# Kernel tuning notes

Hardware: AMD Instinct MI355X
Metric: run time of the kernel (lower is better)

## Reference

```python
import jax, jax.numpy as jnp
import numpy as np

# SectorAttention (PARTNER): dim=256, resolution=(4,4096), H_sp=4, W_sp=1, H=4, heads=8
B, Hq, Hres, Wres, C, NH = 4, 4, 4, 4096, 256, 8
H_SP, W_SP = 4, 1
HD = C // NH
SCALE = HD ** -0.5


def _forward(s, x, s_pos, x_pos, Wq, bq, Wk, bk, Wv, bv, Wo, bo,
             pw1, pb1, bn_g, bn_b, bn_m, bn_v, pw2, pb2,
             ln_g, ln_b, mw1, mb1, mw2, mb2):
    Bb, Lq, Cc = s.shape
    W = Wres
    nW = Bb * (W // W_SP)
    # ---- dynamic relative-position bias (per-window small conv net) ----
    xp = x_pos.reshape(Bb, Hq // H_SP, H_SP, W // W_SP, W_SP, 2)
    xp = jnp.transpose(xp, (0, 1, 3, 5, 2, 4)).reshape(-1, 2, H_SP * W_SP)   # (nW,2,4)
    sp = jnp.transpose(s_pos, (0, 2, 3, 1)).reshape(-1, 2, Hq * W_SP)        # (nW,2,4)
    rel = sp[:, :, :, None] - xp[:, :, None, :]                              # (nW,2,4,4)
    rel = rel.reshape(nW, 2, -1)                                             # (nW,2,16)
    h = jnp.einsum('oc,bcl->bol', pw1, rel) + pb1[None, :, None]             # Conv1d k=1
    h = (h - bn_m[None, :, None]) * jax.lax.rsqrt(bn_v[None, :, None] + 1e-5) \
        * bn_g[None, :, None] + bn_b[None, :, None]                          # BatchNorm1d (eval)
    h = jax.nn.relu(h)
    h = jnp.einsum('oc,bcl->bol', pw2, h) + pb2[None, :, None]               # Conv1d k=1 -> heads
    rel_bias = h.reshape(-1, NH, Hq, H_SP)                                   # (nW,NH,4,4) since W_SP==1
    # ---- projections + window partitioning ----
    q = s @ Wq.T + bq
    q = q.reshape(Bb, Cc, Hq, W)                          # faithful torch .view reinterpretation
    q = q.reshape(Bb, NH, HD, Hq, W // W_SP, W_SP)
    q = jnp.transpose(q, (0, 4, 1, 3, 5, 2)).reshape(-1, NH, Hq * W_SP, HD)

    def im2cswin(t):
        t = jnp.transpose(t, (0, 2, 1)).reshape(Bb, Cc, Hres, W)
        t = t.reshape(Bb, Cc, Hres // H_SP, H_SP, W // W_SP, W_SP)
        t = jnp.transpose(t, (0, 2, 4, 3, 5, 1)).reshape(-1, H_SP * W_SP, Cc)
        return jnp.transpose(t.reshape(-1, H_SP * W_SP, NH, HD), (0, 2, 1, 3))

    k = im2cswin(x @ Wk.T + bk)
    v = im2cswin(x @ Wv.T + bv)
    # ---- windowed attention with dynamic bias ----
    attn = jnp.einsum('wnqd,wnkd->wnqk', q * SCALE, k) + rel_bias
    attn = jax.nn.softmax(attn, axis=-1)
    o = jnp.einsum('wnqk,wnkd->wnqd', attn, v)            # (nW,NH,4,HD)
    o = jnp.transpose(o, (0, 2, 1, 3)).reshape(-1, Hq * W_SP, Cc)
    # windows2img(o, H_sp=Hq, W_sp=W_SP, H=Hq, W=W)
    o = o.reshape(Bb, Hq // Hq, W // W_SP, Hq, W_SP, Cc)
    o = jnp.transpose(o, (0, 1, 3, 2, 4, 5)).reshape(Bb, Hq * W, Cc)
    o = o @ Wo.T + bo
    s1 = s + o
    # ---- LayerNorm + MLP (residual) ----
    mu = jnp.mean(s1, axis=-1, keepdims=True)
    var = jnp.mean((s1 - mu) ** 2, axis=-1, keepdims=True)
    n = (s1 - mu) * jax.lax.rsqrt(var + 1e-5) * ln_g + ln_b
    h2 = jax.nn.gelu(n @ mw1.T + mb1, approximate=False)
    return s1 + h2 @ mw2.T + mb2


def setup_inputs() -> dict:
    key = jax.random.key(0)
    ks = jax.random.split(key, 12)
    rn = lambda k, sh, sc=1.0: jax.random.normal(k, sh, dtype=jnp.float32) * sc
    H4 = 4 * C
    return {
        's': rn(ks[0], (B, Hq * Wres, C)),
        'x': rn(ks[1], (B, Hres * Wres, C)),
        's_pos': rn(ks[2], (B, 2, Wres // W_SP, Hq * W_SP)),
        'x_pos': rn(ks[3], (B, Hres * Wres, 2)),
        'Wq': rn(ks[4], (C, C), 0.02), 'bq': jnp.zeros((C,), jnp.float32),
        'Wk': rn(ks[5], (C, C), 0.02), 'bk': jnp.zeros((C,), jnp.float32),
        'Wv': rn(ks[6], (C, C), 0.02), 'bv': jnp.zeros((C,), jnp.float32),
        'Wo': rn(ks[7], (C, C), 0.02), 'bo': jnp.zeros((C,), jnp.float32),
        'pw1': rn(ks[8], (16, 2), 0.2), 'pb1': jnp.zeros((16,), jnp.float32),
        'bn_g': jnp.ones((16,), jnp.float32), 'bn_b': jnp.zeros((16,), jnp.float32),
        'bn_m': jnp.zeros((16,), jnp.float32), 'bn_v': jnp.ones((16,), jnp.float32),
        'pw2': rn(ks[9], (NH, 16), 0.2), 'pb2': jnp.zeros((NH,), jnp.float32),
        'ln_g': jnp.ones((C,), jnp.float32), 'ln_b': jnp.zeros((C,), jnp.float32),
        'mw1': rn(ks[10], (H4, C), 0.02), 'mb1': jnp.zeros((H4,), jnp.float32),
        'mw2': rn(ks[11], (C, H4), 0.02), 'mb2': jnp.zeros((C,), jnp.float32),
    }


def reference(s, x, s_pos, x_pos, Wq, bq, Wk, bk, Wv, bv, Wo, bo,
              pw1, pb1, bn_g, bn_b, bn_m, bn_v, pw2, pb2,
              ln_g, ln_b, mw1, mb1, mw2, mb2):
    return _forward(s, x, s_pos, x_pos, Wq, bq, Wk, bk, Wv, bv, Wo, bo,
                    pw1, pb1, bn_g, bn_b, bn_m, bn_v, pw2, pb2,
                    ln_g, ln_b, mw1, mb1, mw2, mb2)
```

## Files before the change

kernel.cpp:

```cpp
#include <hip/hip_runtime.h>
#include <hip/hip_bf16.h>
#include <math.h>

typedef __hip_bfloat16 BF;
typedef __bf16 bf16x8 __attribute__((ext_vector_type(8)));
typedef float f32x4 __attribute__((ext_vector_type(4)));

struct alignas(8) BF4 { BF v[4]; };
struct alignas(16) BF8 { BF v[8]; };

static __device__ __forceinline__ float b2f(BF x) { return __bfloat162float(x); }
static __device__ __forceinline__ BF f2b(float x) { return __float2bfloat16(x); }

static __device__ __forceinline__ void gld_lds16(const void* g, void* l) {
  __builtin_amdgcn_global_load_lds(
      (const __attribute__((address_space(1))) unsigned int*)g,
      (__attribute__((address_space(3))) unsigned int*)l, 16, 0, 0);
}

__global__ void __launch_bounds__(256) cvt_kernel(
    const float* __restrict__ in, BF* __restrict__ out, int n4) {
  for (int i = blockIdx.x * 256 + threadIdx.x; i < n4; i += gridDim.x * 256) {
    float4 v = ((const float4*)in)[i];
    BF4 o;
    o.v[0] = f2b(v.x); o.v[1] = f2b(v.y); o.v[2] = f2b(v.z); o.v[3] = f2b(v.w);
    ((BF4*)out)[i] = o;
  }
}

__global__ void __launch_bounds__(256) bkv_kernel(
    const float* __restrict__ bk, const float* __restrict__ bv,
    float* __restrict__ bkv) {
  int i = blockIdx.x * 256 + threadIdx.x;
  bkv[i] = (i < 256) ? bk[i] : bv[i - 256];
}

__global__ void __launch_bounds__(256) bias_kernel(
    const float* __restrict__ s_pos, const float* __restrict__ x_pos,
    const float* __restrict__ pw1, const float* __restrict__ pb1,
    const float* __restrict__ bn_g, const float* __restrict__ bn_b,
    const float* __restrict__ bn_m, const float* __restrict__ bn_v,
    const float* __restrict__ pw2, const float* __restrict__ pb2,
    float* __restrict__ out) {
  int gid = blockIdx.x * 256 + threadIdx.x;
  int w = gid >> 4, l = gid & 15;
  int b = w >> 12, wi = w & 4095;
  int i = l >> 2, j = l & 3;
  int e0 = i, e1 = 4 + i;
  float sp0 = s_pos[(((size_t)b * 2 + (e0 & 1)) * 4096 + wi) * 4 + (e0 >> 1)];
  float sp1 = s_pos[(((size_t)b * 2 + (e1 & 1)) * 4096 + wi) * 4 + (e1 >> 1)];
  float xp0 = x_pos[((size_t)b * 16384 + j * 4096 + wi) * 2 + 0];
  float xp1 = x_pos[((size_t)b * 16384 + j * 4096 + wi) * 2 + 1];
  float r0 = sp0 - xp0, r1 = sp1 - xp1;
  float acc[8];
#pragma unroll
  for (int p = 0; p < 8; ++p) acc[p] = pb2[p];
#pragma unroll
  for (int o = 0; o < 16; ++o) {
    float t = pw1[o * 2 + 0] * r0 + pw1[o * 2 + 1] * r1 + pb1[o];
    float sc = bn_g[o] / sqrtf(bn_v[o] + 1e-5f);
    t = (t - bn_m[o]) * sc + bn_b[o];
    t = fmaxf(t, 0.0f);
#pragma unroll
    for (int p = 0; p < 8; ++p) acc[p] += pw2[p * 16 + o] * t;
  }
#pragma unroll
  for (int p = 0; p < 8; ++p) out[(size_t)w * 128 + p * 16 + l] = acc[p];
}

enum { EPI_NONE = 0, EPI_RES = 1, EPI_GELU = 2 };

template <int EPI, typename AT, typename RT, typename CT>
__global__ void __launch_bounds__(256, 2) gemm_tn(
    const AT* __restrict__ A, const BF* __restrict__ Bw,
    const float* __restrict__ bias, const RT* __restrict__ Res,
    CT* __restrict__ C, int M, int N, int K) {
  constexpr bool F32A = __is_same(AT, float);
  alignas(16) __shared__ BF As[2][8][128][8];
  alignas(16) __shared__ BF Bs[2][8][128][8];
  const int ntiles = N >> 7;
  const int cpx = gridDim.x >> 3;
  const int bid = blockIdx.x;
  const int swz = (bid & 7) * cpx + (bid >> 3);
  const int mt = swz / ntiles, nt = swz % ntiles;
  const int row0 = mt << 7, col0 = nt << 7;
  const int t = threadIdx.x;
  const int wave = t >> 6, lane = t & 63;
  const int wr = wave >> 1, wc = wave & 1;
  const int sm = t & 127;
  const int skc = t >> 7;
  f32x4 acc[4][4] = {};
  const int NT = K >> 6;
  float4 ar[4][2];

  auto stageB = [&](int kt, int dbuf) {
#pragma unroll
    for (int i = 0; i < 4; ++i) {
      const int kc = i * 2 + skc;
      gld_lds16(Bw + (size_t)(col0 + sm) * K + kt * 64 + kc * 8,
                &Bs[dbuf][0][0][0] + (size_t)(i * 256 + wave * 64) * 8);
    }
  };
  auto loadA = [&](int kt) {
    if constexpr (F32A) {
#pragma unroll
      for (int i = 0; i < 4; ++i) {
        const int kc = i * 2 + skc;
        const float* src = A + (size_t)(row0 + sm) * K + kt * 64 + kc * 8;
        ar[i][0] = ((const float4*)src)[0];
        ar[i][1] = ((const float4*)src)[1];
      }
    }
  };
  auto writeA = [&](int dbuf) {
    if constexpr (F32A) {
#pragma unroll
      for (int i = 0; i < 4; ++i) {
        const int kc = i * 2 + skc;
        BF tmp[8];
        tmp[0] = f2b(ar[i][0].x); tmp[1] = f2b(ar[i][0].y);
        tmp[2] = f2b(ar[i][0].z); tmp[3] = f2b(ar[i][0].w);
        tmp[4] = f2b(ar[i][1].x); tmp[5] = f2b(ar[i][1].y);
        tmp[6] = f2b(ar[i][1].z); tmp[7] = f2b(ar[i][1].w);
        *(bf16x8*)(&As[dbuf][kc][sm][0]) = *(bf16x8*)tmp;
      }
    }
  };
  auto stageA_bf = [&](int kt, int dbuf) {
    if constexpr (!F32A) {
#pragma unroll
      for (int i = 0; i < 4; ++i) {
        const int kc = i * 2 + skc;
        gld_lds16((const BF*)A + (size_t)(row0 + sm) * K + kt * 64 + kc * 8,
                  &As[dbuf][0][0][0] + (size_t)(i * 256 + wave * 64) * 8);
      }
    }
  };
  auto compute = [&](int dbuf) {
#pragma unroll
    for (int kk = 0; kk < 2; ++kk) {
      const int chunk = kk * 4 + (lane >> 4);
      const int rl = lane & 15;
      bf16x8 af[4], bfr[4];
#pragma unroll
      for (int mi = 0; mi < 4; ++mi)
        af[mi] = *(const bf16x8*)(&As[dbuf][chunk][wr * 64 + mi * 16 + rl][0]);
#pragma unroll
      for (int ni = 0; ni < 4; ++ni)
        bfr[ni] = *(const bf16x8*)(&Bs[dbuf][chunk][wc * 64 + ni * 16 + rl][0]);
#pragma unroll
      for (int mi = 0; mi < 4; ++mi)
#pragma unroll
        for (int ni = 0; ni < 4; ++ni)
          acc[mi][ni] = __builtin_amdgcn_mfma_f32_16x16x32_bf16(
              af[mi], bfr[ni], acc[mi][ni], 0, 0, 0);
    }
  };

  loadA(0); stageA_bf(0, 0); stageB(0, 0); writeA(0);
  __syncthreads();
  int cur = 0;
  for (int kt = 0; kt < NT; ++kt) {
    const bool more = (kt + 1 < NT);
    if (more) {
      loadA(kt + 1);
      stageA_bf(kt + 1, cur ^ 1);
      stageB(kt + 1, cur ^ 1);
    }
    compute(cur);
    if (more) writeA(cur ^ 1);
    __syncthreads();
    cur ^= 1;
  }

  const int rl = lane & 15, rg = lane >> 4;
#pragma unroll
  for (int mi = 0; mi < 4; ++mi) {
#pragma unroll
    for (int ni = 0; ni < 4; ++ni) {
      const int col = col0 + wc * 64 + ni * 16 + rl;
      const float bcol = bias[col];
#pragma unroll
      for (int r = 0; r < 4; ++r) {
        const int row = row0 + wr * 64 + mi * 16 + rg * 4 + r;
        float v = acc[mi][ni][r] + bcol;
        if constexpr (EPI == EPI_GELU)
          v = 0.5f * v * (1.0f + erff(v * 0.70710678118654752f));
        if constexpr (EPI == EPI_RES) {
          if constexpr (__is_same(RT, float))
            v += Res[(size_t)row * N + col];
          else
            v += b2f(Res[(size_t)row * N + col]);
        }
        if constexpr (__is_same(CT, float))
          C[(size_t)row * N + col] = v;
        else
          C[(size_t)row * N + col] = f2b(v);
      }
    }
  }
}

__global__ void __launch_bounds__(256, 2) gemm_q(
    const float* __restrict__ A, const BF* __restrict__ Bw,
    const float* __restrict__ bias, BF* __restrict__ Qa) {
  constexpr int K = 256;
  alignas(16) __shared__ BF As[2][8][128][8];
  alignas(16) __shared__ BF Bs[2][8][128][8];
  const int cpx = gridDim.x >> 3;
  const int bid = blockIdx.x;
  const int swz = (bid & 7) * cpx + (bid >> 3);
  const int mt = swz >> 1, nt = swz & 1;
  const int hp = mt & 3, qi = (mt >> 2) & 3, nh = (mt >> 4) & 7, bb = mt >> 7;
  const int col0 = nt << 7;
  const int t = threadIdx.x;
  const int wave = t >> 6, lane = t & 63;
  const int wr = wave >> 1, wc = wave & 1;
  const int sm = t & 127;
  const int skc = t >> 7;
  const size_t grow = (size_t)bb * 16384 + nh * 2048 + (size_t)(sm & 31) * 64 +
                      qi * 16 + hp * 4 + (sm >> 5);
  f32x4 acc[4][4] = {};
  float4 ar[4][2];

  auto stageB = [&](int kt, int dbuf) {
#pragma unroll
    for (int i = 0; i < 4; ++i) {
      const int kc = i * 2 + skc;
      gld_lds16(Bw + (size_t)(col0 + sm) * K + kt * 64 + kc * 8,
                &Bs[dbuf][0][0][0] + (size_t)(i * 256 + wave * 64) * 8);
    }
  };
  auto loadA = [&](int kt) {
#pragma unroll
    for (int i = 0; i < 4; ++i) {
      const int kc = i * 2 + skc;
      const float* src = A + grow * K + kt * 64 + kc * 8;
      ar[i][0] = ((const float4*)src)[0];
      ar[i][1] = ((const float4*)src)[1];
    }
  };
  auto writeA = [&](int dbuf) {
#pragma unroll
    for (int i = 0; i < 4; ++i) {
      const int kc = i * 2 + skc;
      BF tmp[8];
      tmp[0] = f2b(ar[i][0].x); tmp[1] = f2b(ar[i][0].y);
      tmp[2] = f2b(ar[i][0].z); tmp[3] = f2b(ar[i][0].w);
      tmp[4] = f2b(ar[i][1].x); tmp[5] = f2b(ar[i][1].y);
      tmp[6] = f2b(ar[i][1].z); tmp[7] = f2b(ar[i][1].w);
      *(bf16x8*)(&As[dbuf][kc][sm][0]) = *(bf16x8*)tmp;
    }
  };
  auto compute = [&](int dbuf) {
#pragma unroll
    for (int kk = 0; kk < 2; ++kk) {
      const int chunk = kk * 4 + (lane >> 4);
      const int rl = lane & 15;
      bf16x8 af[4], bfr[4];
#pragma unroll
      for (int mi = 0; mi < 4; ++mi)
        af[mi] = *(const bf16x8*)(&As[dbuf][chunk][wr * 64 + mi * 16 + rl][0]);
#pragma unroll
      for (int ni = 0; ni < 4; ++ni)
        bfr[ni] = *(const bf16x8*)(&Bs[dbuf][chunk][wc * 64 + ni * 16 + rl][0]);
#pragma unroll
      for (int mi = 0; mi < 4; ++mi)
#pragma unroll
        for (int ni = 0; ni < 4; ++ni)
          acc[mi][ni] = __builtin_amdgcn_mfma_f32_16x16x32_bf16(
              af[mi], bfr[ni], acc[mi][ni], 0, 0, 0);
    }
  };

  loadA(0); stageB(0, 0); writeA(0);
  __syncthreads();
  int cur = 0;
  for (int kt = 0; kt < 4; ++kt) {
    const bool more = (kt + 1 < 4);
    if (more) { loadA(kt + 1); stageB(kt + 1, cur ^ 1); }
    compute(cur);
    if (more) writeA(cur ^ 1);
    __syncthreads();
    cur ^= 1;
  }

  const int rl = lane & 15, rg = lane >> 4;
  const float SCALE = 0.17677669529663689f;
#pragma unroll
  for (int mi = 0; mi < 4; ++mi) {
#pragma unroll
    for (int ni = 0; ni < 4; ++ni) {
      const int col = col0 + wc * 64 + ni * 16 + rl;
      const float bcol = bias[col];
      const int i0 = wr * 64 + mi * 16 + rg * 4;
      const int hd = i0 & 31, hil = i0 >> 5;
      const int wi = (hp * 4 + hil) * 256 + col;
      BF4 pk;
#pragma unroll
      for (int r = 0; r < 4; ++r)
        pk.v[r] = f2b((acc[mi][ni][r] + bcol) * SCALE);
      *(BF4*)(Qa + ((((size_t)bb * 4096 + wi) * 8 + nh) * 128 + qi * 32 + hd)) = pk;
    }
  }
}

__global__ void __launch_bounds__(256) attn_kernel(
    const BF* __restrict__ Qa, const BF* __restrict__ KV,
    const float* __restrict__ biasb, BF* __restrict__ O) {
  const int t = threadIdx.x;
  const int g = t >> 4, l16 = t & 15;
  const int qi = l16 >> 2, kj = l16 & 3;
  const int w = (blockIdx.x << 1) | (g >> 3);
  const int nh = g & 7;
  const int b = w >> 12, wi = w & 4095;

  const uint4* qp = (const uint4*)(Qa + ((((size_t)b * 4096 + wi) * 8 + nh) * 128 + qi * 32));
  uint4 qv[4] = {qp[0], qp[1], qp[2], qp[3]};
  const uint4* kp = (const uint4*)(KV + ((size_t)b * 16384 + kj * 4096 + wi) * 512 + nh * 32);
  uint4 kv[4] = {kp[0], kp[1], kp[2], kp[3]};
  const float bias_l = biasb[(size_t)w * 128 + nh * 16 + l16];
  const BF* vbase = KV + (size_t)b * 16384 * 512 + 256 + nh * 32 + kj * 8;
  uint4 vv[4];
#pragma unroll
  for (int d = 0; d < 4; ++d)
    vv[d] = *(const uint4*)(vbase + ((size_t)((kj ^ d) * 4096 + wi)) * 512);

  float accs[4] = {0.f, 0.f, 0.f, 0.f};
#pragma unroll
  for (int j = 0; j < 4; ++j) {
#pragma unroll
    for (int e = 0; e < 4; ++e) {
      unsigned qe = ((const unsigned*)&qv[j])[e];
      unsigned ke = ((const unsigned*)&kv[j])[e];
      float ql = __uint_as_float(qe << 16);
      float qh = __uint_as_float(qe & 0xffff0000u);
      float kl = __uint_as_float(ke << 16);
      float kh = __uint_as_float(ke & 0xffff0000u);
      accs[e] = fmaf(ql, kl, accs[e]);
      accs[e] = fmaf(qh, kh, accs[e]);
    }
  }
  const float score = accs[0] + accs[1] + accs[2] + accs[3] + bias_l;

  float mx = fmaxf(score, __shfl_xor(score, 1));
  mx = fmaxf(mx, __shfl_xor(mx, 2));
  float e = __expf(score - mx);
  float sm = e + __shfl_xor(e, 1);
  sm += __shfl_xor(sm, 2);
  float p = e / sm;
  float pd[4];
  pd[0] = p;
  pd[1] = __shfl_xor(p, 1);
  pd[2] = __shfl_xor(p, 2);
  pd[3] = __shfl_xor(pd[1], 2);

  float o8[8] = {0.f, 0.f, 0.f, 0.f, 0.f, 0.f, 0.f, 0.f};
#pragma unroll
  for (int d = 0; d < 4; ++d) {
#pragma unroll
    for (int e = 0; e < 4; ++e) {
      unsigned ve = ((const unsigned*)&vv[d])[e];
      o8[e * 2 + 0] = fmaf(pd[d], __uint_as_float(ve << 16), o8[e * 2 + 0]);
      o8[e * 2 + 1] = fmaf(pd[d], __uint_as_float(ve & 0xffff0000u), o8[e * 2 + 1]);
    }
  }
  BF8 ob;
#pragma unroll
  for (int h = 0; h < 8; ++h) ob.v[h] = f2b(o8[h]);
  *(BF8*)(O + ((size_t)b * 16384 + qi * 4096 + wi) * 256 + nh * 32 + kj * 8) = ob;
}

__global__ void __launch_bounds__(256) ln_kernel(
    const BF* __restrict__ S1, const float* __restrict__ g,
    const float* __restrict__ be, BF* __restrict__ Nout) {
  const int wave = threadIdx.x >> 6, lane = threadIdx.x & 63;
  const size_t row = (size_t)blockIdx.x * 4 + wave;
  BF4 d = *(const BF4*)(S1 + row * 256 + lane * 4);
  float x[4] = {b2f(d.v[0]), b2f(d.v[1]), b2f(d.v[2]), b2f(d.v[3])};
  float s = x[0] + x[1] + x[2] + x[3];
  float sq = x[0] * x[0] + x[1] * x[1] + x[2] * x[2] + x[3] * x[3];
#pragma unroll
  for (int m = 1; m <= 32; m <<= 1) {
    s += __shfl_xor(s, m);
    sq += __shfl_xor(sq, m);
  }
  const float mean = s * 0.00390625f;
  const float var = sq * 0.00390625f - mean * mean;
  const float rstd = 1.0f / sqrtf(var + 1e-5f);
  BF4 o;
#pragma unroll
  for (int jj = 0; jj < 4; ++jj) {
    float nv = (x[jj] - mean) * rstd * g[lane * 4 + jj] + be[lane * 4 + jj];
    o.v[jj] = f2b(nv);
  }
  *(BF4*)(Nout + row * 256 + lane * 4) = o;
}

extern "C" void kernel_launch(void* const* d_in, const int* in_sizes, int n_in,
                              void* d_out, int out_size, void* d_ws, size_t ws_size,
                              hipStream_t stream) {
  const float* s     = (const float*)d_in[0];
  const float* x     = (const float*)d_in[1];
  const float* s_pos = (const float*)d_in[2];
  const float* x_pos = (const float*)d_in[3];
  const float* Wq = (const float*)d_in[4];  const float* bq = (const float*)d_in[5];
  const float* Wk = (const float*)d_in[6];  const float* bk = (const float*)d_in[7];
  const float* Wv = (const float*)d_in[8];  const float* bv = (const float*)d_in[9];
  const float* Wo = (const float*)d_in[10]; const float* bo = (const float*)d_in[11];
  const float* pw1 = (const float*)d_in[12]; const float* pb1 = (const float*)d_in[13];
  const float* bn_g = (const float*)d_in[14]; const float* bn_b = (const float*)d_in[15];
  const float* bn_m = (const float*)d_in[16]; const float* bn_v = (const float*)d_in[17];
  const float* pw2 = (const float*)d_in[18]; const float* pb2 = (const float*)d_in[19];
  const float* ln_g = (const float*)d_in[20]; const float* ln_b = (const float*)d_in[21];
  const float* mw1 = (const float*)d_in[22]; const float* mb1 = (const float*)d_in[23];
  const float* mw2 = (const float*)d_in[24]; const float* mb2 = (const float*)d_in[25];

  char* ws = (char*)d_ws;
  float* biasb = (float*)ws;
  BF* Qa   = (BF*)(ws + 8388608);
  BF* KVw  = (BF*)(ws + 41943040);
  BF* S1   = (BF*)(ws + 109051904);
  BF* Wq_bf  = (BF*)(ws + 142606336);
  BF* Wo_bf  = (BF*)(ws + 142737408);
  BF* Wkv_bf = (BF*)(ws + 142868480);
  BF* mw1_bf = (BF*)(ws + 143130624);
  BF* mw2_bf = (BF*)(ws + 143654912);
  float* bkv = (float*)(ws + 144179200);
  BF* Nw = Qa;
  BF* H2 = KVw;
  BF* ObBF = (BF*)d_out;
  float* Of = (float*)d_out;

  cvt_kernel<<<64, 256, 0, stream>>>(Wq, Wq_bf, 16384);
  cvt_kernel<<<64, 256, 0, stream>>>(Wo, Wo_bf, 16384);
  cvt_kernel<<<64, 256, 0, stream>>>(Wk, Wkv_bf, 16384);
  cvt_kernel<<<64, 256, 0, stream>>>(Wv, Wkv_bf + 65536, 16384);
  cvt_kernel<<<256, 256, 0, stream>>>(mw1, mw1_bf, 65536);
  cvt_kernel<<<256, 256, 0, stream>>>(mw2, mw2_bf, 65536);
  bkv_kernel<<<2, 256, 0, stream>>>(bk, bv, bkv);
  bias_kernel<<<1024, 256, 0, stream>>>(s_pos, x_pos, pw1, pb1, bn_g, bn_b,
                                        bn_m, bn_v, pw2, pb2, biasb);

  gemm_q<<<1024, 256, 0, stream>>>(s, Wq_bf, bq, Qa);
  gemm_tn<EPI_NONE, float, float, BF><<<2048, 256, 0, stream>>>(
      x, Wkv_bf, bkv, nullptr, KVw, 65536, 512, 256);
  attn_kernel<<<8192, 256, 0, stream>>>(Qa, KVw, biasb, ObBF);
  gemm_tn<EPI_RES, BF, float, BF><<<1024, 256, 0, stream>>>(
      ObBF, Wo_bf, bo, s, S1, 65536, 256, 256);
  ln_kernel<<<16384, 256, 0, stream>>>(S1, ln_g, ln_b, Nw);
  for (int h = 0; h < 2; ++h) {
    const size_t ro = (size_t)h * 32768;
    gemm_tn<EPI_GELU, BF, float, BF><<<2048, 256, 0, stream>>>(
        Nw + ro * 256, mw1_bf, mb1, nullptr, H2, 32768, 1024, 256);
    gemm_tn<EPI_RES, BF, BF, float><<<512, 256, 0, stream>>>(
        H2, mw2_bf, mb2, S1 + ro * 256, Of + ro * 256, 32768, 256, 1024);
  }
}
```

Measured before the change: 419.9 us.

## Replace double-buffered LDS GEMM pipeline with single buffer and two barriers

Both GEMM kernels drop the second LDS buffer for A and B tiles. The main loop now writes A, stages B, prefetches the next A into registers, syncs, computes, then syncs again. This halves shared memory per block, from 64KB to 32KB, which may allow more resident blocks per CU. The cost is a second barrier per k-step and no overlap between LDS staging and MFMA compute inside a block.

```diff
diff --git a/kernel.cpp b/kernel.cpp
--- a/kernel.cpp
+++ b/kernel.cpp
@@ -76,8 +76,8 @@
     const float* __restrict__ bias, const RT* __restrict__ Res,
     CT* __restrict__ C, int M, int N, int K) {
   constexpr bool F32A = __is_same(AT, float);
-  alignas(16) __shared__ BF As[2][8][128][8];
-  alignas(16) __shared__ BF Bs[2][8][128][8];
+  alignas(16) __shared__ BF As[8][128][8];
+  alignas(16) __shared__ BF Bs[8][128][8];
   const int ntiles = N >> 7;
   const int cpx = gridDim.x >> 3;
   const int bid = blockIdx.x;
@@ -93,12 +93,12 @@
   const int NT = K >> 6;
   float4 ar[4][2];
 
-  auto stageB = [&](int kt, int dbuf) {
+  auto stageB = [&](int kt) {
 #pragma unroll
     for (int i = 0; i < 4; ++i) {
       const int kc = i * 2 + skc;
       gld_lds16(Bw + (size_t)(col0 + sm) * K + kt * 64 + kc * 8,
-                &Bs[dbuf][0][0][0] + (size_t)(i * 256 + wave * 64) * 8);
+                &Bs[0][0][0] + (size_t)(i * 256 + wave * 64) * 8);
     }
   };
   auto loadA = [&](int kt) {
@@ -112,7 +112,7 @@
       }
     }
   };
-  auto writeA = [&](int dbuf) {
+  auto writeA = [&]() {
     if constexpr (F32A) {
 #pragma unroll
       for (int i = 0; i < 4; ++i) {
@@ -122,21 +122,21 @@
         tmp[2] = f2b(ar[i][0].z); tmp[3] = f2b(ar[i][0].w);
         tmp[4] = f2b(ar[i][1].x); tmp[5] = f2b(ar[i][1].y);
         tmp[6] = f2b(ar[i][1].z); tmp[7] = f2b(ar[i][1].w);
-        *(bf16x8*)(&As[dbuf][kc][sm][0]) = *(bf16x8*)tmp;
+        *(bf16x8*)(&As[kc][sm][0]) = *(bf16x8*)tmp;
       }
     }
   };
-  auto stageA_bf = [&](int kt, int dbuf) {
+  auto stageA_bf = [&](int kt) {
     if constexpr (!F32A) {
 #pragma unroll
       for (int i = 0; i < 4; ++i) {
         const int kc = i * 2 + skc;
         gld_lds16((const BF*)A + (size_t)(row0 + sm) * K + kt * 64 + kc * 8,
-                  &As[dbuf][0][0][0] + (size_t)(i * 256 + wave * 64) * 8);
+                  &As[0][0][0] + (size_t)(i * 256 + wave * 64) * 8);
       }
     }
   };
-  auto compute = [&](int dbuf) {
+  auto compute = [&]() {
 #pragma unroll
     for (int kk = 0; kk < 2; ++kk) {
       const int chunk = kk * 4 + (lane >> 4);
@@ -144,10 +144,10 @@
       bf16x8 af[4], bfr[4];
 #pragma unroll
       for (int mi = 0; mi < 4; ++mi)
-        af[mi] = *(const bf16x8*)(&As[dbuf][chunk][wr * 64 + mi * 16 + rl][0]);
+        af[mi] = *(const bf16x8*)(&As[chunk][wr * 64 + mi * 16 + rl][0]);
 #pragma unroll
       for (int ni = 0; ni < 4; ++ni)
-        bfr[ni] = *(const bf16x8*)(&Bs[dbuf][chunk][wc * 64 + ni * 16 + rl][0]);
+        bfr[ni] = *(const bf16x8*)(&Bs[chunk][wc * 64 + ni * 16 + rl][0]);
 #pragma unroll
       for (int mi = 0; mi < 4; ++mi)
 #pragma unroll
@@ -157,20 +157,15 @@
     }
   };
 
-  loadA(0); stageA_bf(0, 0); stageB(0, 0); writeA(0);
-  __syncthreads();
-  int cur = 0;
+  loadA(0);
   for (int kt = 0; kt < NT; ++kt) {
-    const bool more = (kt + 1 < NT);
-    if (more) {
-      loadA(kt + 1);
-      stageA_bf(kt + 1, cur ^ 1);
-      stageB(kt + 1, cur ^ 1);
-    }
-    compute(cur);
-    if (more) writeA(cur ^ 1);
+    writeA();
+    stageA_bf(kt);
+    stageB(kt);
+    if (kt + 1 < NT) loadA(kt + 1);
     __syncthreads();
-    cur ^= 1;
+    compute();
+    __syncthreads();
   }
 
   const int rl = lane & 15, rg = lane >> 4;
@@ -205,8 +200,8 @@
     const float* __restrict__ A, const BF* __restrict__ Bw,
     const float* __restrict__ bias, BF* __restrict__ Qa) {
   constexpr int K = 256;
-  alignas(16) __shared__ BF As[2][8][128][8];
-  alignas(16) __shared__ BF Bs[2][8][128][8];
+  alignas(16) __shared__ BF As[8][128][8];
+  alignas(16) __shared__ BF Bs[8][128][8];
   const int cpx = gridDim.x >> 3;
   const int bid = blockIdx.x;
   const int swz = (bid & 7) * cpx + (bid >> 3);
@@ -223,12 +218,12 @@
   f32x4 acc[4][4] = {};
   float4 ar[4][2];
 
-  auto stageB = [&](int kt, int dbuf) {
+  auto stageB = [&](int kt) {
 #pragma unroll
     for (int i = 0; i < 4; ++i) {
       const int kc = i * 2 + skc;
       gld_lds16(Bw + (size_t)(col0 + sm) * K + kt * 64 + kc * 8,
-                &Bs[dbuf][0][0][0] + (size_t)(i * 256 + wave * 64) * 8);
+                &Bs[0][0][0] + (size_t)(i * 256 + wave * 64) * 8);
     }
   };
   auto loadA = [&](int kt) {
@@ -240,7 +235,7 @@
       ar[i][1] = ((const float4*)src)[1];
     }
   };
-  auto writeA = [&](int dbuf) {
+  auto writeA = [&]() {
 #pragma unroll
     for (int i = 0; i < 4; ++i) {
       const int kc = i * 2 + skc;
@@ -249,10 +244,10 @@
       tmp[2] = f2b(ar[i][0].z); tmp[3] = f2b(ar[i][0].w);
       tmp[4] = f2b(ar[i][1].x); tmp[5] = f2b(ar[i][1].y);
       tmp[6] = f2b(ar[i][1].z); tmp[7] = f2b(ar[i][1].w);
-      *(bf16x8*)(&As[dbuf][kc][sm][0]) = *(bf16x8*)tmp;
-    }
-  };
-  auto compute = [&](int dbuf) {
+      *(bf16x8*)(&As[kc][sm][0]) = *(bf16x8*)tmp;
+    }
+  };
+  auto compute = [&]() {
 #pragma unroll
     for (int kk = 0; kk < 2; ++kk) {
       const int chunk = kk * 4 + (lane >> 4);
@@ -260,10 +255,10 @@
       bf16x8 af[4], bfr[4];
 #pragma unroll
       for (int mi = 0; mi < 4; ++mi)
-        af[mi] = *(const bf16x8*)(&As[dbuf][chunk][wr * 64 + mi * 16 + rl][0]);
+        af[mi] = *(const bf16x8*)(&As[chunk][wr * 64 + mi * 16 + rl][0]);
 #pragma unroll
       for (int ni = 0; ni < 4; ++ni)
-        bfr[ni] = *(const bf16x8*)(&Bs[dbuf][chunk][wc * 64 + ni * 16 + rl][0]);
+        bfr[ni] = *(const bf16x8*)(&Bs[chunk][wc * 64 + ni * 16 + rl][0]);
 #pragma unroll
       for (int mi = 0; mi < 4; ++mi)
 #pragma unroll
@@ -273,16 +268,14 @@
     }
   };
 
-  loadA(0); stageB(0, 0); writeA(0);
-  __syncthreads();
-  int cur = 0;
+  loadA(0);
   for (int kt = 0; kt < 4; ++kt) {
-    const bool more = (kt + 1 < 4);
-    if (more) { loadA(kt + 1); stageB(kt + 1, cur ^ 1); }
-    compute(cur);
-    if (more) writeA(cur ^ 1);
+    writeA();
+    stageB(kt);
+    if (kt + 1 < 4) loadA(kt + 1);
     __syncthreads();
-    cur ^= 1;
+    compute();
+    __syncthreads();
   }
 
   const int rl = lane & 15, rg = lane >> 4;
@@ -359,10 +352,10 @@
 #pragma unroll
   for (int d = 0; d < 4; ++d) {
 #pragma unroll
-    for (int e = 0; e < 4; ++e) {
-      unsigned ve = ((const unsigned*)&vv[d])[e];
-      o8[e * 2 + 0] = fmaf(pd[d], __uint_as_float(ve << 16), o8[e * 2 + 0]);
-      o8[e * 2 + 1] = fmaf(pd[d], __uint_as_float(ve & 0xffff0000u), o8[e * 2 + 1]);
+    for (int e2 = 0; e2 < 4; ++e2) {
+      unsigned ve = ((const unsigned*)&vv[d])[e2];
+      o8[e2 * 2 + 0] = fmaf(pd[d], __uint_as_float(ve << 16), o8[e2 * 2 + 0]);
+      o8[e2 * 2 + 1] = fmaf(pd[d], __uint_as_float(ve & 0xffff0000u), o8[e2 * 2 + 1]);
     }
   }
   BF8 ob;
```

Measured after the change: 401.2 us. 1.05x faster.
